# Kernel optimization log

Measured on AMD Instinct MI355X. Metric: run time of the kernel, lower is better.

The kernel has to match this reference:

```python
import jax, jax.numpy as jnp
import numpy as np

VOCAB = 100000
D = 128
B = 256
L = 2048  # leaves per tree (power of two -> complete binary tree)


def setup_inputs() -> dict:
    key = jax.random.key(0)
    k1, k2, k3, k4 = jax.random.split(key, 4)
    word_ids = jax.random.randint(k1, (B, L), 0, VOCAB)
    embedding = jax.random.normal(k2, (VOCAB, D), dtype=jnp.float32) * 0.1
    # torch nn.Linear(2*D, D): weight [D, 2*D], bias [D]
    W = jax.random.normal(k3, (D, 2 * D), dtype=jnp.float32) * (1.0 / np.sqrt(2 * D))
    b = jax.random.normal(k4, (D,), dtype=jnp.float32) * 0.01
    return {"word_ids": word_ids, "embedding": embedding, "W": W, "b": b}


def reference(word_ids, embedding, W, b):
    # Leaves: embedding lookup for every leaf of every tree. [B, L, D]
    x = embedding[word_ids]
    # Internal nodes, batched by depth: each level combines adjacent pairs
    # via linear(concat(left, right)). log2(L) levels (static unroll).
    while x.shape[1] > 1:
        left = x[:, 0::2, :]   # [B, n/2, D]
        right = x[:, 1::2, :]  # [B, n/2, D]
        pair = jnp.concatenate([left, right], axis=-1)  # [B, n/2, 2D]
        x = jnp.einsum('bnd,od->bno', pair, W) + b      # [B, n/2, D]
    return x[:, 0, :]  # root result per tree, [B, D]
```

## Files before the change

kernel.cpp:

```cpp
#include <hip/hip_runtime.h>


typedef __bf16 bf16x8 __attribute__((ext_vector_type(8)));
typedef __bf16 bf16x4 __attribute__((ext_vector_type(4)));
typedef float f32x4 __attribute__((ext_vector_type(4)));

#define STRIDE 136

__global__ void pack_w_kernel(const float* __restrict__ W,
                              __bf16* __restrict__ wpack) {
    const int f = blockIdx.x;
    const int tid = threadIdx.x;
    const int wv = tid >> 6, l = tid & 63;
    const int nl = f >> 3, kk = f & 7;
    const int o = ((wv << 1) + nl) * 16 + (l & 15);
    const int d = kk * 32 + ((l >> 4) << 3);
    const float* src = W + o * 256 + d;
    bf16x8 h;
#pragma unroll
    for (int j = 0; j < 8; ++j) h[j] = (__bf16)src[j];
    *(bf16x8*)(wpack + (size_t)(f * 256 + tid) * 8) = h;
}

template <int NOUT>
__device__ __forceinline__ void level_step(
    const __bf16* src0, const __bf16* src1, __bf16* dst,
    const bf16x8* wf, const float* bval, int wv, int q, int lm)
{
    const int ntm = (NOUT + 15) >> 4;
#pragma unroll
    for (int mt = 0; mt < ntm; ++mt) {
        const __bf16* src = mt ? src1 : src0;
        const int me = (NOUT >= 16) ? lm : (lm < NOUT ? lm : 0);
        bf16x8 af[8];
#pragma unroll
        for (int kk = 0; kk < 8; ++kk) {
            const int hi = kk >> 2;
            const int col = (kk & 3) * 32 + q * 8;
            const int row = 2 * me + hi;
            af[kk] = *(const bf16x8*)&src[row * STRIDE + col];
        }
#pragma unroll
        for (int nl = 0; nl < 2; ++nl) {
            f32x4 acc = { bval[nl], bval[nl], bval[nl], bval[nl] };
#pragma unroll
            for (int kk = 0; kk < 8; ++kk)
                acc = __builtin_amdgcn_mfma_f32_16x16x32_bf16(
                    af[kk], wf[nl * 8 + kk], acc, 0, 0, 0);
            const int col = (2 * wv + nl) * 16 + lm;
            const bf16x4 hv = __builtin_convertvector(acc, bf16x4);
#pragma unroll
            for (int r = 0; r < 4; ++r) {
                const int row = mt * 16 + q * 4 + r;
                if (row < NOUT)
                    dst[row * STRIDE + col] = hv[r];
            }
        }
    }
    __syncthreads();
}

__device__ __forceinline__ void level_final(
    const __bf16* src, __bf16* yrow,
    const bf16x8* wf, const float* bval, int wv, int q, int lm)
{
    const int me = (lm < 2) ? lm : 0;
    bf16x8 af[8];
#pragma unroll
    for (int kk = 0; kk < 8; ++kk) {
        const int hi = kk >> 2;
        const int col = (kk & 3) * 32 + q * 8;
        af[kk] = *(const bf16x8*)&src[(2 * me + hi) * STRIDE + col];
    }
#pragma unroll
    for (int nl = 0; nl < 2; ++nl) {
        f32x4 acc = { bval[nl], bval[nl], bval[nl], bval[nl] };
#pragma unroll
        for (int kk = 0; kk < 8; ++kk)
            acc = __builtin_amdgcn_mfma_f32_16x16x32_bf16(
                af[kk], wf[nl * 8 + kk], acc, 0, 0, 0);
        const int col = (2 * wv + nl) * 16 + lm;
        if (q == 0) {
            yrow[0 * 128 + col] = (__bf16)acc[0];
            yrow[1 * 128 + col] = (__bf16)acc[1];
        }
    }
}

__global__ __launch_bounds__(256, 3) void tree128_kernel(
    const int* __restrict__ wid, const float* __restrict__ emb,
    const __bf16* __restrict__ wpack, const float* __restrict__ bias,
    __bf16* __restrict__ yout)
{
    __shared__ __align__(16) __bf16 bufA[128 * STRIDE];
    __shared__ __align__(16) __bf16 bufB[32 * STRIDE];
    const int tid = threadIdx.x;
    const int batch = blockIdx.x >> 4;
    const int grp = blockIdx.x & 15;
    const int wv = tid >> 6, ln = tid & 63, q = ln >> 4, lm = ln & 15;

    bf16x8 wf[16];
    const bf16x8* wp = (const bf16x8*)wpack;
#pragma unroll
    for (int f = 0; f < 16; ++f) wf[f] = wp[f * 256 + tid];
    float bval[2];
    bval[0] = bias[(2 * wv + 0) * 16 + lm];
    bval[1] = bias[(2 * wv + 1) * 16 + lm];

    const int* wb = wid + batch * 2048 + grp * 128;
    int idreg[16];
#pragma unroll
    for (int i = 0; i < 16; ++i) idreg[i] = wb[(tid >> 5) + 8 * i];

#pragma unroll
    for (int i = 0; i < 16; ++i) {
        const int row = (tid >> 5) + 8 * i;
        const int c4 = tid & 31;
        const f32x4 v = *(const f32x4*)(emb + (size_t)idreg[i] * 128 + c4 * 4);
        *(bf16x4*)&bufA[row * STRIDE + c4 * 4] =
            __builtin_convertvector(v, bf16x4);
    }
    __syncthreads();

    __bf16* A = bufA;
    __bf16* B = bufB;
    level_step<32>(A,               A + 32 * STRIDE, B,              wf, bval, wv, q, lm);
    level_step<32>(A + 64 * STRIDE, A + 96 * STRIDE, A,              wf, bval, wv, q, lm);
    level_step<32>(B,               A,               A + 32 * STRIDE,wf, bval, wv, q, lm);
    level_step<16>(A + 32 * STRIDE, nullptr,         B,              wf, bval, wv, q, lm);
    level_step<8> (B,               nullptr,         A,              wf, bval, wv, q, lm);
    level_step<4> (A,               nullptr,         B,              wf, bval, wv, q, lm);
    level_final(B, yout + (size_t)(batch * 32 + grp * 2) * 128,
                wf, bval, wv, q, lm);
}

__global__ __launch_bounds__(256) void tree32_kernel(
    const __bf16* __restrict__ yin, const __bf16* __restrict__ wpack,
    const float* __restrict__ bias, float* __restrict__ out)
{
    __shared__ __align__(16) __bf16 buf[2][32 * STRIDE];
    const int tid = threadIdx.x;
    const int batch = blockIdx.x;
    const int wv = tid >> 6, ln = tid & 63, q = ln >> 4, lm = ln & 15;

    bf16x8 wf[16];
    const bf16x8* wp = (const bf16x8*)wpack;
#pragma unroll
    for (int f = 0; f < 16; ++f) wf[f] = wp[f * 256 + tid];
    float bval[2];
    bval[0] = bias[(2 * wv + 0) * 16 + lm];
    bval[1] = bias[(2 * wv + 1) * 16 + lm];

#pragma unroll
    for (int i = 0; i < 2; ++i) {
        const int flat = tid + 256 * i;
        const int row = flat >> 4;
        const int c8 = flat & 15;
        const bf16x8 v =
            *(const bf16x8*)(yin + (size_t)(batch * 32 + row) * 128 + c8 * 8);
        *(bf16x8*)&buf[0][row * STRIDE + c8 * 8] = v;
    }
    __syncthreads();

    int nin = 32, rb = 0;
    while (nin > 1) {
        const int nout = nin >> 1;
        const int me = (lm < nout) ? lm : 0;
        bf16x8 af[8];
#pragma unroll
        for (int kk = 0; kk < 8; ++kk) {
            const int hi = kk >> 2;
            const int col = (kk & 3) * 32 + q * 8;
            af[kk] = *(const bf16x8*)&buf[rb][(2 * me + hi) * STRIDE + col];
        }
#pragma unroll
        for (int nl = 0; nl < 2; ++nl) {
            f32x4 acc = { bval[nl], bval[nl], bval[nl], bval[nl] };
#pragma unroll
            for (int kk = 0; kk < 8; ++kk)
                acc = __builtin_amdgcn_mfma_f32_16x16x32_bf16(
                    af[kk], wf[nl * 8 + kk], acc, 0, 0, 0);
            const int col = (2 * wv + nl) * 16 + lm;
            if (nout == 1) {
                if (q == 0) out[(size_t)batch * 128 + col] = acc[0];
            } else {
                const bf16x4 hv = __builtin_convertvector(acc, bf16x4);
#pragma unroll
                for (int r = 0; r < 4; ++r) {
                    const int row = q * 4 + r;
                    if (row < nout)
                        buf[rb ^ 1][row * STRIDE + col] = hv[r];
                }
            }
        }
        __syncthreads();
        rb ^= 1;
        nin = nout;
    }
}

extern "C" void kernel_launch(void* const* d_in, const int* in_sizes, int n_in,
                              void* d_out, int out_size, void* d_ws, size_t ws_size,
                              hipStream_t stream) {
    const int*   wid = (const int*)d_in[0];
    const float* emb = (const float*)d_in[1];
    const float* W   = (const float*)d_in[2];
    const float* b   = (const float*)d_in[3];
    float* out = (float*)d_out;

    __bf16* wpack = (__bf16*)d_ws;
    __bf16* y     = wpack + 32768;

    pack_w_kernel<<<16, 256, 0, stream>>>(W, wpack);
    tree128_kernel<<<4096, 256, 0, stream>>>(wid, emb, wpack, b, y);
    tree32_kernel<<<256, 256, 0, stream>>>(y, wpack, b, out);
}
```

Baseline: 131.0 us.

## Halve tree128 LDS by gathering leaves in two halves, raise occupancy target

The leaf gather in tree128_kernel is split into two 64-row halves. The first half is reduced into bufB before the second half is gathered into the same buffer. This cuts shared memory per block from about 160 rows to 128 rows of bf16 and raises the launch-bounds block target from 3 to 4 per CU. The MFMA inner loops now interleave A-fragment loads in two k-halves with two accumulators, lowering the live registers for A fragments, and tree32 unrolls its level loop into the templated steps. The cost is an extra barrier between the gathers and serialised gather latency inside each block.

Measured after the change: 128.4 us. 2.0% less time.

```diff
diff --git a/kernel.cpp b/kernel.cpp
--- a/kernel.cpp
+++ b/kernel.cpp
@@ -32,23 +32,27 @@
     for (int mt = 0; mt < ntm; ++mt) {
         const __bf16* src = mt ? src1 : src0;
         const int me = (NOUT >= 16) ? lm : (lm < NOUT ? lm : 0);
-        bf16x8 af[8];
-#pragma unroll
-        for (int kk = 0; kk < 8; ++kk) {
-            const int hi = kk >> 2;
-            const int col = (kk & 3) * 32 + q * 8;
-            const int row = 2 * me + hi;
-            af[kk] = *(const bf16x8*)&src[row * STRIDE + col];
+        f32x4 acc[2];
+        acc[0] = f32x4{ bval[0], bval[0], bval[0], bval[0] };
+        acc[1] = f32x4{ bval[1], bval[1], bval[1], bval[1] };
+#pragma unroll
+        for (int kh = 0; kh < 2; ++kh) {
+            const int row = 2 * me + kh;
+            bf16x8 af[4];
+#pragma unroll
+            for (int j = 0; j < 4; ++j)
+                af[j] = *(const bf16x8*)&src[row * STRIDE + j * 32 + q * 8];
+#pragma unroll
+            for (int nl = 0; nl < 2; ++nl)
+#pragma unroll
+                for (int j = 0; j < 4; ++j)
+                    acc[nl] = __builtin_amdgcn_mfma_f32_16x16x32_bf16(
+                        af[j], wf[nl * 8 + kh * 4 + j], acc[nl], 0, 0, 0);
         }
 #pragma unroll
         for (int nl = 0; nl < 2; ++nl) {
-            f32x4 acc = { bval[nl], bval[nl], bval[nl], bval[nl] };
-#pragma unroll
-            for (int kk = 0; kk < 8; ++kk)
-                acc = __builtin_amdgcn_mfma_f32_16x16x32_bf16(
-                    af[kk], wf[nl * 8 + kk], acc, 0, 0, 0);
             const int col = (2 * wv + nl) * 16 + lm;
-            const bf16x4 hv = __builtin_convertvector(acc, bf16x4);
+            const bf16x4 hv = __builtin_convertvector(acc[nl], bf16x4);
 #pragma unroll
             for (int r = 0; r < 4; ++r) {
                 const int row = mt * 16 + q * 4 + r;
@@ -65,35 +69,56 @@
     const bf16x8* wf, const float* bval, int wv, int q, int lm)
 {
     const int me = (lm < 2) ? lm : 0;
-    bf16x8 af[8];
-#pragma unroll
-    for (int kk = 0; kk < 8; ++kk) {
-        const int hi = kk >> 2;
-        const int col = (kk & 3) * 32 + q * 8;
-        af[kk] = *(const bf16x8*)&src[(2 * me + hi) * STRIDE + col];
+    f32x4 acc[2];
+    acc[0] = f32x4{ bval[0], bval[0], bval[0], bval[0] };
+    acc[1] = f32x4{ bval[1], bval[1], bval[1], bval[1] };
+#pragma unroll
+    for (int kh = 0; kh < 2; ++kh) {
+        const int row = 2 * me + kh;
+        bf16x8 af[4];
+#pragma unroll
+        for (int j = 0; j < 4; ++j)
+            af[j] = *(const bf16x8*)&src[row * STRIDE + j * 32 + q * 8];
+#pragma unroll
+        for (int nl = 0; nl < 2; ++nl)
+#pragma unroll
+            for (int j = 0; j < 4; ++j)
+                acc[nl] = __builtin_amdgcn_mfma_f32_16x16x32_bf16(
+                    af[j], wf[nl * 8 + kh * 4 + j], acc[nl], 0, 0, 0);
     }
 #pragma unroll
     for (int nl = 0; nl < 2; ++nl) {
-        f32x4 acc = { bval[nl], bval[nl], bval[nl], bval[nl] };
-#pragma unroll
-        for (int kk = 0; kk < 8; ++kk)
-            acc = __builtin_amdgcn_mfma_f32_16x16x32_bf16(
-                af[kk], wf[nl * 8 + kk], acc, 0, 0, 0);
         const int col = (2 * wv + nl) * 16 + lm;
         if (q == 0) {
-            yrow[0 * 128 + col] = (__bf16)acc[0];
-            yrow[1 * 128 + col] = (__bf16)acc[1];
-        }
-    }
-}
-
-__global__ __launch_bounds__(256, 3) void tree128_kernel(
+            yrow[0 * 128 + col] = (__bf16)acc[nl][0];
+            yrow[1 * 128 + col] = (__bf16)acc[nl][1];
+        }
+    }
+}
+
+__device__ __forceinline__ void gather64(
+    const int* wb64, const float* emb, __bf16* dstA, int tid)
+{
+    int idreg[8];
+#pragma unroll
+    for (int i = 0; i < 8; ++i) idreg[i] = wb64[(tid >> 5) + 8 * i];
+#pragma unroll
+    for (int i = 0; i < 8; ++i) {
+        const int row = (tid >> 5) + 8 * i;
+        const int c4 = tid & 31;
+        const f32x4 v = *(const f32x4*)(emb + (size_t)idreg[i] * 128 + c4 * 4);
+        *(bf16x4*)&dstA[row * STRIDE + c4 * 4] =
+            __builtin_convertvector(v, bf16x4);
+    }
+}
+
+__global__ __launch_bounds__(256, 4) void tree128_kernel(
     const int* __restrict__ wid, const float* __restrict__ emb,
     const __bf16* __restrict__ wpack, const float* __restrict__ bias,
     __bf16* __restrict__ yout)
 {
-    __shared__ __align__(16) __bf16 bufA[128 * STRIDE];
-    __shared__ __align__(16) __bf16 bufB[32 * STRIDE];
+    __shared__ __align__(16) __bf16 bufA[64 * STRIDE];
+    __shared__ __align__(16) __bf16 bufB[64 * STRIDE];
     const int tid = threadIdx.x;
     const int batch = blockIdx.x >> 4;
     const int grp = blockIdx.x & 15;
@@ -108,29 +133,20 @@
     bval[1] = bias[(2 * wv + 1) * 16 + lm];
 
     const int* wb = wid + batch * 2048 + grp * 128;
-    int idreg[16];
-#pragma unroll
-    for (int i = 0; i < 16; ++i) idreg[i] = wb[(tid >> 5) + 8 * i];
-
-#pragma unroll
-    for (int i = 0; i < 16; ++i) {
-        const int row = (tid >> 5) + 8 * i;
-        const int c4 = tid & 31;
-        const f32x4 v = *(const f32x4*)(emb + (size_t)idreg[i] * 128 + c4 * 4);
-        *(bf16x4*)&bufA[row * STRIDE + c4 * 4] =
-            __builtin_convertvector(v, bf16x4);
-    }
-    __syncthreads();
-
-    __bf16* A = bufA;
-    __bf16* B = bufB;
-    level_step<32>(A,               A + 32 * STRIDE, B,              wf, bval, wv, q, lm);
-    level_step<32>(A + 64 * STRIDE, A + 96 * STRIDE, A,              wf, bval, wv, q, lm);
-    level_step<32>(B,               A,               A + 32 * STRIDE,wf, bval, wv, q, lm);
-    level_step<16>(A + 32 * STRIDE, nullptr,         B,              wf, bval, wv, q, lm);
-    level_step<8> (B,               nullptr,         A,              wf, bval, wv, q, lm);
-    level_step<4> (A,               nullptr,         B,              wf, bval, wv, q, lm);
-    level_final(B, yout + (size_t)(batch * 32 + grp * 2) * 128,
+
+    gather64(wb, emb, bufA, tid);
+    __syncthreads();
+    level_step<32>(bufA, bufA + 32 * STRIDE, bufB,
+                   wf, bval, wv, q, lm);
+    gather64(wb + 64, emb, bufA, tid);
+    __syncthreads();
+    level_step<32>(bufA, bufA + 32 * STRIDE, bufB + 32 * STRIDE,
+                   wf, bval, wv, q, lm);
+    level_step<32>(bufB, bufB + 32 * STRIDE, bufA, wf, bval, wv, q, lm);
+    level_step<16>(bufA, nullptr,            bufB, wf, bval, wv, q, lm);
+    level_step<8> (bufB, nullptr,            bufA, wf, bval, wv, q, lm);
+    level_step<4> (bufA, nullptr,            bufB, wf, bval, wv, q, lm);
+    level_final(bufB, yout + (size_t)(batch * 32 + grp * 2) * 128,
                 wf, bval, wv, q, lm);
 }
 
@@ -138,7 +154,8 @@
     const __bf16* __restrict__ yin, const __bf16* __restrict__ wpack,
     const float* __restrict__ bias, float* __restrict__ out)
 {
-    __shared__ __align__(16) __bf16 buf[2][32 * STRIDE];
+    __shared__ __align__(16) __bf16 buf0[32 * STRIDE];
+    __shared__ __align__(16) __bf16 buf1[16 * STRIDE];
     const int tid = threadIdx.x;
     const int batch = blockIdx.x;
     const int wv = tid >> 6, ln = tid & 63, q = ln >> 4, lm = ln & 15;
@@ -158,44 +175,37 @@
         const int c8 = flat & 15;
         const bf16x8 v =
             *(const bf16x8*)(yin + (size_t)(batch * 32 + row) * 128 + c8 * 8);
-        *(bf16x8*)&buf[0][row * STRIDE + c8 * 8] = v;
-    }
-    __syncthreads();
-
-    int nin = 32, rb = 0;
-    while (nin > 1) {
-        const int nout = nin >> 1;
-        const int me = (lm < nout) ? lm : 0;
-        bf16x8 af[8];
-#pragma unroll
-        for (int kk = 0; kk < 8; ++kk) {
-            const int hi = kk >> 2;
-            const int col = (kk & 3) * 32 + q * 8;
-            af[kk] = *(const bf16x8*)&buf[rb][(2 * me + hi) * STRIDE + col];
+        *(bf16x8*)&buf0[row * STRIDE + c8 * 8] = v;
+    }
+    __syncthreads();
+
+    level_step<16>(buf0, nullptr, buf1, wf, bval, wv, q, lm);
+    level_step<8> (buf1, nullptr, buf0, wf, bval, wv, q, lm);
+    level_step<4> (buf0, nullptr, buf1, wf, bval, wv, q, lm);
+    level_step<2> (buf1, nullptr, buf0, wf, bval, wv, q, lm);
+
+    {
+        f32x4 acc[2];
+        acc[0] = f32x4{ bval[0], bval[0], bval[0], bval[0] };
+        acc[1] = f32x4{ bval[1], bval[1], bval[1], bval[1] };
+#pragma unroll
+        for (int kh = 0; kh < 2; ++kh) {
+            bf16x8 af[4];
+#pragma unroll
+            for (int j = 0; j < 4; ++j)
+                af[j] = *(const bf16x8*)&buf0[kh * STRIDE + j * 32 + q * 8];
+#pragma unroll
+            for (int nl = 0; nl < 2; ++nl)
+#pragma unroll
+                for (int j = 0; j < 4; ++j)
+                    acc[nl] = __builtin_amdgcn_mfma_f32_16x16x32_bf16(
+                        af[j], wf[nl * 8 + kh * 4 + j], acc[nl], 0, 0, 0);
         }
 #pragma unroll
         for (int nl = 0; nl < 2; ++nl) {
-            f32x4 acc = { bval[nl], bval[nl], bval[nl], bval[nl] };
-#pragma unroll
-            for (int kk = 0; kk < 8; ++kk)
-                acc = __builtin_amdgcn_mfma_f32_16x16x32_bf16(
-                    af[kk], wf[nl * 8 + kk], acc, 0, 0, 0);
             const int col = (2 * wv + nl) * 16 + lm;
-            if (nout == 1) {
-                if (q == 0) out[(size_t)batch * 128 + col] = acc[0];
-            } else {
-                const bf16x4 hv = __builtin_convertvector(acc, bf16x4);
-#pragma unroll
-                for (int r = 0; r < 4; ++r) {
-                    const int row = q * 4 + r;
-                    if (row < nout)
-                        buf[rb ^ 1][row * STRIDE + col] = hv[r];
-                }
-            }
-        }
-        __syncthreads();
-        rb ^= 1;
-        nin = nout;
+            if (q == 0) out[(size_t)batch * 128 + col] = acc[nl][0];
+        }
     }
 }
 
```
